# Kernel tuning notes

Hardware: AMD Instinct MI355X
Metric: run time of the kernel (lower is better)

## Reference

```python
import jax, jax.numpy as jnp
import numpy as np

N, E, F_IN, HEADS, C_HEAD, HID, B, NCLS = 20000, 320000, 128, 2, 256, 512, 64, 38
EL = E + N  # edges with self-loops appended


def _bn(x, g, b, eps=1e-5):
    mu = jnp.mean(x, 0)
    var = jnp.mean((x - mu) ** 2, 0)
    return g * (x - mu) * jax.lax.rsqrt(var + eps) + b


def _gcn(x, W, b, src, dst):
    # src/dst already include self-loops; symmetric deg^-1/2 normalization (PyG GCNConv)
    h = x @ W                                             # [N, HID]
    deg = jax.ops.segment_sum(jnp.ones(EL, x.dtype), dst, N)
    norm = jax.lax.rsqrt(jnp.maximum(deg, 1.0))
    coef = norm[src] * norm[dst]                          # [EL]
    agg = jax.ops.segment_sum(h[src] * coef[:, None], dst, N)
    return agg + b


def _gat(x, W, a_src, a_dst, b, src, dst):
    # PyG GATConv, heads=2, concat: alpha = softmax_dst(leaky_relu(a_s.h_src + a_d.h_dst))
    h = (x @ W).reshape(N, HEADS, C_HEAD)
    as_n = jnp.sum(h * a_src, -1)                         # [N, HEADS]
    ad_n = jnp.sum(h * a_dst, -1)
    e = jax.nn.leaky_relu(as_n[src] + ad_n[dst], 0.2)     # [EL, HEADS]
    m = jax.ops.segment_max(e, dst, N)
    ex = jnp.exp(e - m[dst])
    s = jax.ops.segment_sum(ex, dst, N)
    alpha = ex / s[dst]                                   # [EL, HEADS]
    out = jax.ops.segment_sum(h[src] * alpha[:, :, None], dst, N)
    return out.reshape(N, HEADS * C_HEAD) + b


def setup_inputs() -> dict:
    key = jax.random.key(0)
    ks = jax.random.split(key, 40)
    x = jax.random.normal(ks[0], (N, F_IN), jnp.float32)
    edge_index = jax.random.randint(ks[1], (2, E), 0, N, jnp.int32)
    batch = jnp.sort(jax.random.randint(ks[2], (N,), 0, B, jnp.int32))

    def lin(k, fi, fo):
        bound = np.sqrt(6.0 / fi)
        return jax.random.uniform(k, (fi, fo), jnp.float32, -bound, bound)

    d = dict(x=x, edge_index=edge_index, batch=batch)
    # feature transform
    d['ft_W'] = lin(ks[3], F_IN, HID); d['ft_b'] = jnp.zeros(HID)
    d['ft_g'] = jnp.ones(HID); d['ft_be'] = jnp.zeros(HID)
    # GCN block
    d['gcn1_W'] = lin(ks[4], HID, HID); d['gcn1_b'] = jnp.zeros(HID)
    d['gbn1_g'] = jnp.ones(HID); d['gbn1_b'] = jnp.zeros(HID)
    d['gcn2_W'] = lin(ks[5], HID, HID); d['gcn2_b'] = jnp.zeros(HID)
    d['gbn2_g'] = jnp.ones(HID); d['gbn2_b'] = jnp.zeros(HID)
    # GAT block
    abound = np.sqrt(6.0 / HEADS)
    d['gat1_W'] = lin(ks[6], HID, HID)
    d['gat1_as'] = jax.random.uniform(ks[7], (HEADS, C_HEAD), jnp.float32, -abound, abound)
    d['gat1_ad'] = jax.random.uniform(ks[8], (HEADS, C_HEAD), jnp.float32, -abound, abound)
    d['gat1_b'] = jnp.zeros(HID)
    d['abn1_g'] = jnp.ones(HID); d['abn1_b'] = jnp.zeros(HID)
    d['gat2_W'] = lin(ks[9], HID, HID)
    d['gat2_as'] = jax.random.uniform(ks[10], (HEADS, C_HEAD), jnp.float32, -abound, abound)
    d['gat2_ad'] = jax.random.uniform(ks[11], (HEADS, C_HEAD), jnp.float32, -abound, abound)
    d['gat2_b'] = jnp.zeros(HID)
    d['abn2_g'] = jnp.ones(HID); d['abn2_b'] = jnp.zeros(HID)
    # classifier
    d['fc1_W'] = lin(ks[12], 2 * HID, HID); d['fc1_b'] = jnp.zeros(HID)
    d['cbn1_g'] = jnp.ones(HID); d['cbn1_b'] = jnp.zeros(HID)
    d['fc2_W'] = lin(ks[13], HID, HID // 2); d['fc2_b'] = jnp.zeros(HID // 2)
    d['cbn2_g'] = jnp.ones(HID // 2); d['cbn2_b'] = jnp.zeros(HID // 2)
    d['out_W'] = lin(ks[14], HID // 2, NCLS); d['out_b'] = jnp.zeros(NCLS)
    return d


def reference(x, edge_index, batch,
              ft_W, ft_b, ft_g, ft_be,
              gcn1_W, gcn1_b, gbn1_g, gbn1_b, gcn2_W, gcn2_b, gbn2_g, gbn2_b,
              gat1_W, gat1_as, gat1_ad, gat1_b, abn1_g, abn1_b,
              gat2_W, gat2_as, gat2_ad, gat2_b, abn2_g, abn2_b,
              fc1_W, fc1_b, cbn1_g, cbn1_b, fc2_W, fc2_b, cbn2_g, cbn2_b,
              out_W, out_b):
    loop = jnp.arange(N, dtype=edge_index.dtype)
    src = jnp.concatenate([edge_index[0], loop])
    dst = jnp.concatenate([edge_index[1], loop])

    # feature transform: Linear -> BN -> LeakyReLU(0.2)
    h = jax.nn.leaky_relu(_bn(x @ ft_W + ft_b, ft_g, ft_be), 0.2)
    # GCN block
    h = jax.nn.elu(_bn(_gcn(h, gcn1_W, gcn1_b, src, dst), gbn1_g, gbn1_b))
    h = jax.nn.elu(_bn(_gcn(h, gcn2_W, gcn2_b, src, dst), gbn2_g, gbn2_b))
    # GAT block
    h = jax.nn.elu(_bn(_gat(h, gat1_W, gat1_as, gat1_ad, gat1_b, src, dst), abn1_g, abn1_b))
    h = jax.nn.elu(_bn(_gat(h, gat2_W, gat2_as, gat2_ad, gat2_b, src, dst), abn2_g, abn2_b))
    # global mean+max pool over graphs
    cnt = jax.ops.segment_sum(jnp.ones(N, h.dtype), batch, B)
    mean_p = jax.ops.segment_sum(h, batch, B) / jnp.maximum(cnt, 1.0)[:, None]
    max_p = jax.ops.segment_max(h, batch, B)
    p = jnp.concatenate([mean_p, max_p], axis=1)           # [B, 1024]
    # classifier: fc1 -> bn -> fc2 -> bn -> leaky_relu -> out
    z = _bn(p @ fc1_W + fc1_b, cbn1_g, cbn1_b)
    z = _bn(z @ fc2_W + fc2_b, cbn2_g, cbn2_b)
    z = jax.nn.leaky_relu(z, 0.2)
    return z @ out_W + out_b                                # [B, NCLS]
```

## Files before the change

kernel.cpp:

```cpp
#include <hip/hip_runtime.h>

#define N_NODES 20000
#define N_EDGES 320000
#define EDG_ALL (N_EDGES + N_NODES)
#define F_IN 128
#define HID 512
#define NB 64
#define NCLS 38
#define M_PAD2 20480
#define ROW_BLKS 160
#define NBLK_SCAN ((N_NODES + 255) / 256)
#define BN_ROWS 16
#define BN_GRID ((N_NODES + BN_ROWS - 1) / BN_ROWS)
#define NPART 64
#define POOL_SPLIT 4

typedef short bf16x8 __attribute__((ext_vector_type(8)));
typedef float f32x4 __attribute__((ext_vector_type(4)));
typedef _Float16 f16;
typedef _Float16 f16x2 __attribute__((ext_vector_type(2)));
typedef _Float16 f16x8 __attribute__((ext_vector_type(8)));

__device__ inline unsigned short f2bf(float f) {
  union { float f; unsigned u; } v; v.f = f;
  unsigned r = v.u + 0x7FFF + ((v.u >> 16) & 1);
  return (unsigned short)(r >> 16);
}

__device__ inline void split2(float f, unsigned short& h, unsigned short& l) {
  unsigned short hh = f2bf(f);
  union { unsigned u; float f; } vh; vh.u = ((unsigned)hh) << 16;
  h = hh;
  l = f2bf(f - vh.f);
}

__device__ inline void gload16(const void* g, void* l) {
  __builtin_amdgcn_global_load_lds(
      (const __attribute__((address_space(1))) unsigned int*)g,
      (__attribute__((address_space(3))) unsigned int*)l, 16, 0, 0);
}

__device__ inline float lrelu(float v) { return v > 0.f ? v : 0.2f * v; }


__global__ void deg_count(const int* __restrict__ ei, int* __restrict__ deg) {
  int e = blockIdx.x * blockDim.x + threadIdx.x;
  if (e >= EDG_ALL) return;
  int d = (e < N_EDGES) ? ei[N_EDGES + e] : (e - N_EDGES);
  atomicAdd(&deg[d], 1);
}

__global__ void scan_p1(const int* __restrict__ deg, int* __restrict__ bsum) {
  __shared__ int sh[256];
  int b = blockIdx.x, t = threadIdx.x, i = b * 256 + t;
  sh[t] = (i < N_NODES) ? deg[i] : 0;
  __syncthreads();
  for (int o = 128; o > 0; o >>= 1) {
    if (t < o) sh[t] += sh[t + o];
    __syncthreads();
  }
  if (t == 0) bsum[b] = sh[0];
}

__global__ void scan_p2(const int* __restrict__ bsum, int* __restrict__ boff) {
  __shared__ int sh[128];
  int t = threadIdx.x;
  sh[t] = (t < NBLK_SCAN) ? bsum[t] : 0;
  __syncthreads();
  for (int o = 1; o < 128; o <<= 1) {
    int v = (t >= o) ? sh[t - o] : 0;
    __syncthreads();
    sh[t] += v;
    __syncthreads();
  }
  boff[t] = (t == 0) ? 0 : sh[t - 1];
}

__global__ void scan_p3(const int* __restrict__ deg, const int* __restrict__ boff,
                        int* __restrict__ row_ptr) {
  __shared__ int sh[256];
  int b = blockIdx.x, t = threadIdx.x, i = b * 256 + t;
  sh[t] = (i < N_NODES) ? deg[i] : 0;
  __syncthreads();
  for (int o = 1; o < 256; o <<= 1) {
    int v = (t >= o) ? sh[t - o] : 0;
    __syncthreads();
    sh[t] += v;
    __syncthreads();
  }
  if (i < N_NODES) row_ptr[i + 1] = boff[b] + sh[t];
  if (i == 0) row_ptr[0] = 0;
}

__global__ void compute_norm(const int* __restrict__ deg, float* __restrict__ norm) {
  int i = blockIdx.x * blockDim.x + threadIdx.x;
  if (i >= N_NODES) return;
  norm[i] = rsqrtf(fmaxf((float)deg[i], 1.f));
}

__global__ void fill_csr(const int* __restrict__ ei, int* __restrict__ cursor,
                         int* __restrict__ csr_src) {
  int e = blockIdx.x * blockDim.x + threadIdx.x;
  if (e >= EDG_ALL) return;
  int s, d;
  if (e < N_EDGES) { s = ei[e]; d = ei[N_EDGES + e]; }
  else { s = d = e - N_EDGES; }
  int pos = atomicAdd(&cursor[d], 1);
  csr_src[pos] = s;
}


__global__ void conv_split4(const float* __restrict__ in, unsigned short* __restrict__ hi,
                            unsigned short* __restrict__ lo, int n4) {
  int i = blockIdx.x * blockDim.x + threadIdx.x;
  if (i >= n4) return;
  float4 v = ((const float4*)in)[i];
  ushort4 h, l;
  split2(v.x, h.x, l.x); split2(v.y, h.y, l.y);
  split2(v.z, h.z, l.z); split2(v.w, h.w, l.w);
  ((ushort4*)hi)[i] = h;
  ((ushort4*)lo)[i] = l;
}

__global__ __launch_bounds__(256) void wtrans_split(const float* __restrict__ W,
                                                    unsigned short* __restrict__ WTh,
                                                    unsigned short* __restrict__ WTl,
                                                    int K, int N) {
  __shared__ float sh[32][33];
  int k0 = blockIdx.y * 32, n0 = blockIdx.x * 32;
  int r = threadIdx.x >> 5, c = threadIdx.x & 31;
#pragma unroll
  for (int i = 0; i < 4; ++i)
    sh[r + 8 * i][c] = W[(size_t)(k0 + r + 8 * i) * N + n0 + c];
  __syncthreads();
#pragma unroll
  for (int i = 0; i < 4; ++i) {
    unsigned short h, l;
    split2(sh[c][r + 8 * i], h, l);
    WTh[(size_t)(n0 + r + 8 * i) * K + k0 + c] = h;
    WTl[(size_t)(n0 + r + 8 * i) * K + k0 + c] = l;
  }
}

__global__ __launch_bounds__(256) void ftrans(const float* __restrict__ W,
                                              float* __restrict__ WT, int K, int N) {
  __shared__ float sh[32][33];
  int k0 = blockIdx.y * 32, n0 = blockIdx.x * 32;
  int r = threadIdx.x >> 5, c = threadIdx.x & 31;
#pragma unroll
  for (int i = 0; i < 4; ++i) {
    int k = k0 + r + 8 * i, n = n0 + c;
    sh[r + 8 * i][c] = (k < K && n < N) ? W[(size_t)k * N + n] : 0.f;
  }
  __syncthreads();
#pragma unroll
  for (int i = 0; i < 4; ++i) {
    int n = n0 + r + 8 * i, k = k0 + c;
    if (n < N && k < K) WT[(size_t)n * K + k] = sh[c][r + 8 * i];
  }
}


template <int K, typename OT>
__global__ __launch_bounds__(256) void mm_split(const unsigned short* __restrict__ Ah,
                                                const unsigned short* __restrict__ Al,
                                                const unsigned short* __restrict__ Bh,
                                                const unsigned short* __restrict__ Bl,
                                                const float* __restrict__ bias,
                                                OT* __restrict__ C) {
  __shared__ unsigned short AsH[4096], AsL[4096], BsH[4096], BsL[4096];
  const int t = threadIdx.x;
  const int wid = t >> 6, l = t & 63;
  const int bid = blockIdx.x;
  const int g = bid >> 5, w = bid & 31;
  const int row0 = (g * 8 + (w & 7)) * 128;
  const int col0 = (w >> 3) * 128;
  const int wm = wid >> 1, wn = wid & 1;

  f32x4 acc[4][4];
#pragma unroll
  for (int m = 0; m < 4; ++m)
#pragma unroll
    for (int n = 0; n < 4; ++n)
#pragma unroll
      for (int q = 0; q < 4; ++q) acc[m][n][q] = 0.f;

  const size_t aoff = (size_t)(row0 + wid * 32 + (l >> 2)) * K + (l & 3) * 8;
  const size_t boff = (size_t)(col0 + wid * 32 + (l >> 2)) * K + (l & 3) * 8;
  const unsigned short* gAh0 = Ah + aoff; const unsigned short* gAh1 = gAh0 + (size_t)16 * K;
  const unsigned short* gAl0 = Al + aoff; const unsigned short* gAl1 = gAl0 + (size_t)16 * K;
  const unsigned short* gBh0 = Bh + boff; const unsigned short* gBh1 = gBh0 + (size_t)16 * K;
  const unsigned short* gBl0 = Bl + boff; const unsigned short* gBl1 = gBl0 + (size_t)16 * K;
  unsigned short* lAh0 = &AsH[(wid * 2 + 0) * 512];
  unsigned short* lAh1 = &AsH[(wid * 2 + 1) * 512];
  unsigned short* lAl0 = &AsL[(wid * 2 + 0) * 512];
  unsigned short* lAl1 = &AsL[(wid * 2 + 1) * 512];
  unsigned short* lBh0 = &BsH[(wid * 2 + 0) * 512];
  unsigned short* lBh1 = &BsH[(wid * 2 + 1) * 512];
  unsigned short* lBl0 = &BsL[(wid * 2 + 0) * 512];
  unsigned short* lBl1 = &BsL[(wid * 2 + 1) * 512];

  const int lr = l & 15, kq = (l >> 4) * 8;

  for (int kt = 0; kt < K / 32; ++kt) {
    const int ko = kt * 32;
    gload16(gAh0 + ko, lAh0);
    gload16(gAh1 + ko, lAh1);
    gload16(gAl0 + ko, lAl0);
    gload16(gAl1 + ko, lAl1);
    gload16(gBh0 + ko, lBh0);
    gload16(gBh1 + ko, lBh1);
    gload16(gBl0 + ko, lBl0);
    gload16(gBl1 + ko, lBl1);
    __syncthreads();
    bf16x8 ah[4], al[4], bh[4], bl[4];
#pragma unroll
    for (int m = 0; m < 4; ++m) {
      int ro = (wm * 64 + m * 16 + lr) * 32 + kq;
      ah[m] = *(const bf16x8*)&AsH[ro];
      al[m] = *(const bf16x8*)&AsL[ro];
    }
#pragma unroll
    for (int n = 0; n < 4; ++n) {
      int ro = (wn * 64 + n * 16 + lr) * 32 + kq;
      bh[n] = *(const bf16x8*)&BsH[ro];
      bl[n] = *(const bf16x8*)&BsL[ro];
    }
#pragma unroll
    for (int m = 0; m < 4; ++m)
#pragma unroll
      for (int n = 0; n < 4; ++n) {
        acc[m][n] = __builtin_amdgcn_mfma_f32_16x16x32_bf16(ah[m], bh[n], acc[m][n], 0, 0, 0);
        acc[m][n] = __builtin_amdgcn_mfma_f32_16x16x32_bf16(al[m], bh[n], acc[m][n], 0, 0, 0);
        acc[m][n] = __builtin_amdgcn_mfma_f32_16x16x32_bf16(ah[m], bl[n], acc[m][n], 0, 0, 0);
      }
    __syncthreads();
  }

  const int lg = l >> 4;
#pragma unroll
  for (int m = 0; m < 4; ++m) {
    int row = row0 + wm * 64 + m * 16 + lg * 4;
#pragma unroll
    for (int n = 0; n < 4; ++n) {
      int col = col0 + wn * 64 + n * 16 + lr;
      float bv = bias ? bias[col] : 0.f;
#pragma unroll
      for (int j = 0; j < 4; ++j)
        C[(size_t)(row + j) * HID + col] = (OT)(acc[m][n][j] + bv);
    }
  }
}


__global__ __launch_bounds__(256) void colstats(const f16* __restrict__ X, int n,
                                                float* __restrict__ part) {
  int t = threadIdx.x;
  int r0 = blockIdx.x * BN_ROWS;
  int r1 = min(r0 + BN_ROWS, n);
  float s0 = 0, q0 = 0, s1 = 0, q1 = 0;
  const f16x2* X2 = (const f16x2*)X;
  for (int r = r0; r < r1; ++r) {
    f16x2 v = X2[(size_t)r * 256 + t];
    float a = (float)v.x, b = (float)v.y;
    s0 += a; q0 += a * a;
    s1 += b; q1 += b * b;
  }
  float* pb = part + (size_t)(blockIdx.x & (NPART - 1)) * 1024;
  atomicAdd(&pb[2 * t], s0);
  atomicAdd(&pb[2 * t + 1], s1);
  atomicAdd(&pb[HID + 2 * t], q0);
  atomicAdd(&pb[HID + 2 * t + 1], q1);
}

__global__ __launch_bounds__(256) void stats_comb(const float* __restrict__ part,
                                                  float* __restrict__ stats) {
  int j = blockIdx.x * 256 + threadIdx.x;
  float s = 0.f;
#pragma unroll 8
  for (int k = 0; k < NPART; ++k) s += part[(size_t)k * 1024 + j];
  stats[j] = s;
}

__global__ __launch_bounds__(256) void bn_act(f16* __restrict__ X, int n,
                                              const float* __restrict__ stats,
                                              const float* __restrict__ g,
                                              const float* __restrict__ b, int act,
                                              unsigned short* __restrict__ hio,
                                              unsigned short* __restrict__ loo,
                                              int writeX) {
  int t = threadIdx.x;
  int r0 = blockIdx.x * BN_ROWS;
  int r1 = min(r0 + BN_ROWS, n);
  float invn = 1.f / (float)n;
  float mu0 = stats[2 * t] * invn, mu1 = stats[2 * t + 1] * invn;
  float v0 = stats[HID + 2 * t] * invn - mu0 * mu0;
  float v1 = stats[HID + 2 * t + 1] * invn - mu1 * mu1;
  float2 gg = ((const float2*)g)[t];
  float2 bb = ((const float2*)b)[t];
  float sc0 = gg.x * rsqrtf(v0 + 1e-5f);
  float sc1 = gg.y * rsqrtf(v1 + 1e-5f);
  f16x2* X2 = (f16x2*)X;
  ushort2* H2 = (ushort2*)hio;
  ushort2* L2p = (ushort2*)loo;
  for (int r = r0; r < r1; ++r) {
    f16x2 xv = X2[(size_t)r * 256 + t];
    float y0 = sc0 * ((float)xv.x - mu0) + bb.x;
    float y1 = sc1 * ((float)xv.y - mu1) + bb.y;
    if (act == 1) {
      y0 = y0 > 0.f ? y0 : 0.2f * y0;
      y1 = y1 > 0.f ? y1 : 0.2f * y1;
    } else {
      y0 = y0 > 0.f ? y0 : expm1f(y0);
      y1 = y1 > 0.f ? y1 : expm1f(y1);
    }
    unsigned short h0, l0, h1, l1;
    split2(y0, h0, l0);
    split2(y1, h1, l1);
    ushort2 hh; hh.x = h0; hh.y = h1;
    ushort2 ll; ll.x = l0; ll.y = l1;
    H2[(size_t)r * 256 + t] = hh;
    L2p[(size_t)r * 256 + t] = ll;
    if (writeX) {
      f16x2 yv; yv.x = (f16)y0; yv.y = (f16)y1;
      X2[(size_t)r * 256 + t] = yv;
    }
  }
}


__global__ __launch_bounds__(256) void gcn_agg_w(
    const f16* __restrict__ h, const int* __restrict__ row_ptr,
    const int* __restrict__ csr_src, const float* __restrict__ norm,
    const float* __restrict__ bias, f16* __restrict__ out) {
  int node = blockIdx.x * 4 + (threadIdx.x >> 6);
  int l = threadIdx.x & 63;
  int beg = row_ptr[node], end = row_ptr[node + 1];
  float ni = norm[node];
  const f16x8* h8 = (const f16x8*)h;
  float acc[8] = {};
  int e = beg;
  for (; e + 4 <= end; e += 4) {
    int s0 = csr_src[e], s1 = csr_src[e + 1], s2 = csr_src[e + 2], s3 = csr_src[e + 3];
    float c0 = norm[s0] * ni, c1 = norm[s1] * ni, c2 = norm[s2] * ni, c3 = norm[s3] * ni;
    f16x8 v0 = h8[(size_t)s0 * 64 + l];
    f16x8 v1 = h8[(size_t)s1 * 64 + l];
    f16x8 v2 = h8[(size_t)s2 * 64 + l];
    f16x8 v3 = h8[(size_t)s3 * 64 + l];
#pragma unroll
    for (int k = 0; k < 8; ++k)
      acc[k] += c0 * (float)v0[k] + c1 * (float)v1[k] + c2 * (float)v2[k] + c3 * (float)v3[k];
  }
  for (; e < end; ++e) {
    int s = csr_src[e];
    float c = norm[s] * ni;
    f16x8 v = h8[(size_t)s * 64 + l];
#pragma unroll
    for (int k = 0; k < 8; ++k) acc[k] += c * (float)v[k];
  }
  float4 b0 = ((const float4*)bias)[l * 2];
  float4 b1 = ((const float4*)bias)[l * 2 + 1];
  f16x8 o;
  o[0] = (f16)(acc[0] + b0.x); o[1] = (f16)(acc[1] + b0.y);
  o[2] = (f16)(acc[2] + b0.z); o[3] = (f16)(acc[3] + b0.w);
  o[4] = (f16)(acc[4] + b1.x); o[5] = (f16)(acc[5] + b1.y);
  o[6] = (f16)(acc[6] + b1.z); o[7] = (f16)(acc[7] + b1.w);
  ((f16x8*)out)[(size_t)node * 64 + l] = o;
}


__device__ inline float wave_sum(float v) {
#pragma unroll
  for (int o = 32; o > 0; o >>= 1) v += __shfl_down(v, o);
  return v;
}

__global__ __launch_bounds__(256) void gat_prep_h(
    const f16* __restrict__ h, const float* __restrict__ a_src,
    const float* __restrict__ a_dst, float* __restrict__ asn, float* __restrict__ adn) {
  int i = blockIdx.x;
  int t = threadIdx.x;
  f16x2 hv = ((const f16x2*)h)[(size_t)i * 256 + t];
  float2 as2 = ((const float2*)a_src)[t];
  float2 ad2 = ((const float2*)a_dst)[t];
  float h0 = (float)hv.x, h1 = (float)hv.y;
  float s = h0 * as2.x + h1 * as2.y;
  float d = h0 * ad2.x + h1 * ad2.y;
  s = wave_sum(s); d = wave_sum(d);
  __shared__ float red[4][2];
  int w = t >> 6;
  if ((t & 63) == 0) { red[w][0] = s; red[w][1] = d; }
  __syncthreads();
  if (t == 0) {
    asn[2 * i]     = red[0][0] + red[1][0];
    asn[2 * i + 1] = red[2][0] + red[3][0];
    adn[2 * i]     = red[0][1] + red[1][1];
    adn[2 * i + 1] = red[2][1] + red[3][1];
  }
}

__global__ __launch_bounds__(256) void gat_agg_w(
    const f16* __restrict__ h, const int* __restrict__ row_ptr,
    const int* __restrict__ csr_src, const float* __restrict__ asn,
    const float* __restrict__ adn, const float* __restrict__ bias,
    f16* __restrict__ out) {
  int node = blockIdx.x * 4 + (threadIdx.x >> 6);
  int l = threadIdx.x & 63;
  int hl = l & 31;
  int hd = (l >> 5) & 1;
  int beg = row_ptr[node], end = row_ptr[node + 1];
  float aD = adn[2 * node + hd];

  float m = -3.4e38f;
  for (int e = beg + hl; e < end; e += 32) {
    int s = csr_src[e];
    m = fmaxf(m, lrelu(asn[2 * s + hd] + aD));
  }
#pragma unroll
  for (int o = 16; o > 0; o >>= 1) m = fmaxf(m, __shfl_xor(m, o));
  float M = m;

  const f16x8* h8 = (const f16x8*)h;
  float acc[8] = {};
  float sw = 0.f;
  int e = beg;
  for (; e + 4 <= end; e += 4) {
    int s0 = csr_src[e], s1 = csr_src[e + 1], s2 = csr_src[e + 2], s3 = csr_src[e + 3];
    float u0 = expf(lrelu(asn[2 * s0 + hd] + aD) - M);
    float u1 = expf(lrelu(asn[2 * s1 + hd] + aD) - M);
    float u2 = expf(lrelu(asn[2 * s2 + hd] + aD) - M);
    float u3 = expf(lrelu(asn[2 * s3 + hd] + aD) - M);
    sw += u0 + u1 + u2 + u3;
    f16x8 v0 = h8[(size_t)s0 * 64 + l];
    f16x8 v1 = h8[(size_t)s1 * 64 + l];
    f16x8 v2 = h8[(size_t)s2 * 64 + l];
    f16x8 v3 = h8[(size_t)s3 * 64 + l];
#pragma unroll
    for (int k = 0; k < 8; ++k)
      acc[k] += u0 * (float)v0[k] + u1 * (float)v1[k] + u2 * (float)v2[k] + u3 * (float)v3[k];
  }
  for (; e < end; ++e) {
    int s = csr_src[e];
    float u = expf(lrelu(asn[2 * s + hd] + aD) - M);
    sw += u;
    f16x8 v = h8[(size_t)s * 64 + l];
#pragma unroll
    for (int k = 0; k < 8; ++k) acc[k] += u * (float)v[k];
  }
  float iS = 1.f / sw;
  float4 b0 = ((const float4*)bias)[l * 2];
  float4 b1 = ((const float4*)bias)[l * 2 + 1];
  f16x8 o;
  o[0] = (f16)(acc[0] * iS + b0.x); o[1] = (f16)(acc[1] * iS + b0.y);
  o[2] = (f16)(acc[2] * iS + b0.z); o[3] = (f16)(acc[3] * iS + b0.w);
  o[4] = (f16)(acc[4] * iS + b1.x); o[5] = (f16)(acc[5] * iS + b1.y);
  o[6] = (f16)(acc[6] * iS + b1.z); o[7] = (f16)(acc[7] * iS + b1.w);
  ((f16x8*)out)[(size_t)node * 64 + l] = o;
}


__global__ void graph_starts(const int* __restrict__ batch, int* __restrict__ start) {
  int i = blockIdx.x * blockDim.x + threadIdx.x;
  if (i >= N_NODES) return;
  int b = batch[i];
  int bp = (i == 0) ? -1 : batch[i - 1];
  for (int g = bp + 1; g <= b; ++g) start[g] = i;
  if (i == N_NODES - 1) {
    for (int g = b + 1; g <= NB; ++g) start[g] = N_NODES;
  }
}

__global__ __launch_bounds__(256) void pool_part(const f16* __restrict__ h,
                                                 const int* __restrict__ start,
                                                 float* __restrict__ pp_sum,
                                                 float* __restrict__ pp_max) {
  int b = blockIdx.x, ch = blockIdx.y, t = threadIdx.x;
  int s = start[b], e = start[b + 1];
  int len = e - s;
  int c0 = s + (len * ch) / POOL_SPLIT;
  int c1 = s + (len * (ch + 1)) / POOL_SPLIT;
  const f16x2* h2 = (const f16x2*)h;
  float s0 = 0.f, s1 = 0.f, m0 = -3.4e38f, m1 = -3.4e38f;
  int r = c0;
  for (; r + 2 <= c1; r += 2) {
    f16x2 v0 = h2[(size_t)(r + 0) * 256 + t];
    f16x2 v1 = h2[(size_t)(r + 1) * 256 + t];
    float a0 = (float)v0.x, a1 = (float)v0.y, b0 = (float)v1.x, b1 = (float)v1.y;
    s0 += a0 + b0; s1 += a1 + b1;
    m0 = fmaxf(m0, fmaxf(a0, b0));
    m1 = fmaxf(m1, fmaxf(a1, b1));
  }
  for (; r < c1; ++r) {
    f16x2 v = h2[(size_t)r * 256 + t];
    float a0 = (float)v.x, a1 = (float)v.y;
    s0 += a0; s1 += a1;
    m0 = fmaxf(m0, a0); m1 = fmaxf(m1, a1);
  }
  size_t base = ((size_t)b * POOL_SPLIT + ch) * HID;
  pp_sum[base + 2 * t] = s0;
  pp_sum[base + 2 * t + 1] = s1;
  pp_max[base + 2 * t] = m0;
  pp_max[base + 2 * t + 1] = m1;
}

__global__ __launch_bounds__(512) void pool_comb(const float* __restrict__ pp_sum,
                                                 const float* __restrict__ pp_max,
                                                 const int* __restrict__ start,
                                                 float* __restrict__ p) {
  int b = blockIdx.x, t = threadIdx.x;
  float sum = 0.f, mx = -3.4e38f;
#pragma unroll
  for (int ch = 0; ch < POOL_SPLIT; ++ch) {
    sum += pp_sum[((size_t)b * POOL_SPLIT + ch) * HID + t];
    mx = fmaxf(mx, pp_max[((size_t)b * POOL_SPLIT + ch) * HID + t]);
  }
  float cnt = (float)(start[b + 1] - start[b]);
  p[b * 1024 + t] = sum / fmaxf(cnt, 1.f);
  p[b * 1024 + 512 + t] = mx;
}


__global__ __launch_bounds__(256) void fc_wave(const float* __restrict__ A,
                                               const float* __restrict__ WT,
                                               const float* __restrict__ bias,
                                               float* __restrict__ C, int K, int Ncol) {
  int r = blockIdx.x;
  int wid = threadIdx.x >> 6, l = threadIdx.x & 63;
  int c = blockIdx.y * 4 + wid;
  if (c >= Ncol) return;
  const float* a = A + (size_t)r * K;
  const float* w = WT + (size_t)c * K;
  float s = 0.f;
  for (int k = l; k < K; k += 64) s += a[k] * w[k];
#pragma unroll
  for (int o = 32; o > 0; o >>= 1) s += __shfl_down(s, o);
  if (l == 0) C[(size_t)r * Ncol + c] = s + bias[c];
}

__global__ void bn_small(float* __restrict__ X, int R, int C,
                         const float* __restrict__ g, const float* __restrict__ b, int act) {
  int c = blockIdx.x * blockDim.x + threadIdx.x;
  if (c >= C) return;
  float s = 0.f, q = 0.f;
  for (int r = 0; r < R; ++r) {
    float v = X[r * C + c];
    s += v; q += v * v;
  }
  float mu = s / R;
  float var = q / R - mu * mu;
  float sc = g[c] * rsqrtf(var + 1e-5f);
  float bb = b[c];
  for (int r = 0; r < R; ++r) {
    float v = sc * (X[r * C + c] - mu) + bb;
    if (act == 1) v = v > 0.f ? v : 0.2f * v;
    X[r * C + c] = v;
  }
}


extern "C" void kernel_launch(void* const* d_in, const int* in_sizes, int n_in,
                              void* d_out, int out_size, void* d_ws, size_t ws_size,
                              hipStream_t stream) {
  const float* x      = (const float*)d_in[0];
  const int*   ei     = (const int*)d_in[1];
  const int*   batch  = (const int*)d_in[2];
  const float* ft_W   = (const float*)d_in[3];
  const float* ft_b   = (const float*)d_in[4];
  const float* ft_g   = (const float*)d_in[5];
  const float* ft_be  = (const float*)d_in[6];
  const float* gcn1_W = (const float*)d_in[7];
  const float* gcn1_b = (const float*)d_in[8];
  const float* gbn1_g = (const float*)d_in[9];
  const float* gbn1_b = (const float*)d_in[10];
  const float* gcn2_W = (const float*)d_in[11];
  const float* gcn2_b = (const float*)d_in[12];
  const float* gbn2_g = (const float*)d_in[13];
  const float* gbn2_b = (const float*)d_in[14];
  const float* gat1_W = (const float*)d_in[15];
  const float* gat1_as= (const float*)d_in[16];
  const float* gat1_ad= (const float*)d_in[17];
  const float* gat1_b = (const float*)d_in[18];
  const float* abn1_g = (const float*)d_in[19];
  const float* abn1_b = (const float*)d_in[20];
  const float* gat2_W = (const float*)d_in[21];
  const float* gat2_as= (const float*)d_in[22];
  const float* gat2_ad= (const float*)d_in[23];
  const float* gat2_b = (const float*)d_in[24];
  const float* abn2_g = (const float*)d_in[25];
  const float* abn2_b = (const float*)d_in[26];
  const float* fc1_W  = (const float*)d_in[27];
  const float* fc1_b  = (const float*)d_in[28];
  const float* cbn1_g = (const float*)d_in[29];
  const float* cbn1_b = (const float*)d_in[30];
  const float* fc2_W  = (const float*)d_in[31];
  const float* fc2_b  = (const float*)d_in[32];
  const float* cbn2_g = (const float*)d_in[33];
  const float* cbn2_b = (const float*)d_in[34];
  const float* out_W  = (const float*)d_in[35];
  const float* out_b  = (const float*)d_in[36];

  char* ws = (char*)d_ws;
  size_t off = 0;
  auto alloc = [&](size_t bytes) -> void* {
    void* p = ws + off;
    off = (off + bytes + 255) & ~(size_t)255;
    return p;
  };

  float* buf0 = (float*)alloc((size_t)M_PAD2 * HID * 4);
  float* buf1 = (float*)alloc((size_t)M_PAD2 * HID * 4);
  unsigned short* ahi = (unsigned short*)alloc((size_t)M_PAD2 * HID * 2);
  unsigned short* alo = (unsigned short*)alloc((size_t)M_PAD2 * HID * 2);
  unsigned short* wh_ft = (unsigned short*)alloc((size_t)HID * F_IN * 2);
  unsigned short* wl_ft = (unsigned short*)alloc((size_t)HID * F_IN * 2);
  unsigned short* wh_g1 = (unsigned short*)alloc((size_t)HID * HID * 2);
  unsigned short* wl_g1 = (unsigned short*)alloc((size_t)HID * HID * 2);
  unsigned short* wh_g2 = (unsigned short*)alloc((size_t)HID * HID * 2);
  unsigned short* wl_g2 = (unsigned short*)alloc((size_t)HID * HID * 2);
  unsigned short* wh_a1 = (unsigned short*)alloc((size_t)HID * HID * 2);
  unsigned short* wl_a1 = (unsigned short*)alloc((size_t)HID * HID * 2);
  unsigned short* wh_a2 = (unsigned short*)alloc((size_t)HID * HID * 2);
  unsigned short* wl_a2 = (unsigned short*)alloc((size_t)HID * HID * 2);
  float* fc1t = (float*)alloc((size_t)512 * 1024 * 4);
  float* fc2t = (float*)alloc((size_t)256 * 512 * 4);
  float* outt = (float*)alloc((size_t)NCLS * 256 * 4);
  int*   row_ptr = (int*)alloc((N_NODES + 1) * 4);
  int*   cursor  = (int*)alloc(N_NODES * 4);
  int*   deg     = (int*)alloc(N_NODES * 4);
  int*   csr_src = (int*)alloc(EDG_ALL * 4);
  float* norm    = (float*)alloc(N_NODES * 4);
  float* asn     = (float*)alloc(N_NODES * 2 * 4);
  float* adn     = (float*)alloc(N_NODES * 2 * 4);
  float* stats   = (float*)alloc(1024 * 4);
  float* spart   = (float*)alloc((size_t)NPART * 1024 * 4);
  int*   bsum    = (int*)alloc(128 * 4);
  int*   boff    = (int*)alloc(128 * 4);
  int*   start   = (int*)alloc((NB + 1) * 4);
  float* p       = (float*)alloc(NB * 1024 * 4);
  float* pp_sum  = (float*)alloc((size_t)NB * POOL_SPLIT * HID * 4);
  float* pp_max  = (float*)alloc((size_t)NB * POOL_SPLIT * HID * 4);
  float* z1      = (float*)alloc(NB * HID * 4);
  float* z2      = (float*)alloc(NB * 256 * 4);
  unsigned short* xhi = (unsigned short*)buf0;
  unsigned short* xlo = xhi + (size_t)M_PAD2 * F_IN;
  f16* xbuf = (f16*)buf0;
  f16* hbuf = (f16*)buf1;

  const dim3 blk256(256);
  const dim3 mmGrid(ROW_BLKS * 4);
  const int aggGrid = N_NODES / 4;

#define BN_BLOCK(XBUF, G, B, ACT, WX)                                            \
  hipMemsetAsync(spart, 0, (size_t)NPART * 1024 * 4, stream);                    \
  colstats<<<BN_GRID, blk256, 0, stream>>>(XBUF, N_NODES, spart);                \
  stats_comb<<<4, blk256, 0, stream>>>(spart, stats);                            \
  bn_act<<<BN_GRID, blk256, 0, stream>>>(XBUF, N_NODES, stats, G, B, ACT, ahi, alo, WX);

  hipMemsetAsync(deg, 0, N_NODES * 4, stream);
  deg_count<<<(EDG_ALL + 255) / 256, blk256, 0, stream>>>(ei, deg);
  scan_p1<<<NBLK_SCAN, blk256, 0, stream>>>(deg, bsum);
  scan_p2<<<1, 128, 0, stream>>>(bsum, boff);
  scan_p3<<<NBLK_SCAN, blk256, 0, stream>>>(deg, boff, row_ptr);
  compute_norm<<<(N_NODES + 255) / 256, blk256, 0, stream>>>(deg, norm);
  hipMemcpyAsync(cursor, row_ptr, N_NODES * 4, hipMemcpyDeviceToDevice, stream);
  fill_csr<<<(EDG_ALL + 255) / 256, blk256, 0, stream>>>(ei, cursor, csr_src);

  wtrans_split<<<dim3(HID / 32, F_IN / 32), blk256, 0, stream>>>(ft_W, wh_ft, wl_ft, F_IN, HID);
  wtrans_split<<<dim3(HID / 32, HID / 32), blk256, 0, stream>>>(gcn1_W, wh_g1, wl_g1, HID, HID);
  wtrans_split<<<dim3(HID / 32, HID / 32), blk256, 0, stream>>>(gcn2_W, wh_g2, wl_g2, HID, HID);
  wtrans_split<<<dim3(HID / 32, HID / 32), blk256, 0, stream>>>(gat1_W, wh_a1, wl_a1, HID, HID);
  wtrans_split<<<dim3(HID / 32, HID / 32), blk256, 0, stream>>>(gat2_W, wh_a2, wl_a2, HID, HID);
  ftrans<<<dim3(512 / 32, 1024 / 32), blk256, 0, stream>>>(fc1_W, fc1t, 1024, 512);
  ftrans<<<dim3(256 / 32, 512 / 32), blk256, 0, stream>>>(fc2_W, fc2t, 512, 256);
  ftrans<<<dim3((NCLS + 31) / 32, 256 / 32), blk256, 0, stream>>>(out_W, outt, 256, NCLS);

  conv_split4<<<(N_NODES * F_IN / 4 + 255) / 256, blk256, 0, stream>>>(x, xhi, xlo, N_NODES * F_IN / 4);
  mm_split<F_IN, f16><<<mmGrid, blk256, 0, stream>>>(xhi, xlo, wh_ft, wl_ft, ft_b, hbuf);
  BN_BLOCK(hbuf, ft_g, ft_be, 1, 0)

  mm_split<HID, f16><<<mmGrid, blk256, 0, stream>>>(ahi, alo, wh_g1, wl_g1, nullptr, hbuf);
  gcn_agg_w<<<aggGrid, blk256, 0, stream>>>(hbuf, row_ptr, csr_src, norm, gcn1_b, xbuf);
  BN_BLOCK(xbuf, gbn1_g, gbn1_b, 2, 0)

  mm_split<HID, f16><<<mmGrid, blk256, 0, stream>>>(ahi, alo, wh_g2, wl_g2, nullptr, hbuf);
  gcn_agg_w<<<aggGrid, blk256, 0, stream>>>(hbuf, row_ptr, csr_src, norm, gcn2_b, xbuf);
  BN_BLOCK(xbuf, gbn2_g, gbn2_b, 2, 0)

  mm_split<HID, f16><<<mmGrid, blk256, 0, stream>>>(ahi, alo, wh_a1, wl_a1, nullptr, hbuf);
  gat_prep_h<<<N_NODES, blk256, 0, stream>>>(hbuf, gat1_as, gat1_ad, asn, adn);
  gat_agg_w<<<aggGrid, blk256, 0, stream>>>(hbuf, row_ptr, csr_src, asn, adn, gat1_b, xbuf);
  BN_BLOCK(xbuf, abn1_g, abn1_b, 2, 0)

  mm_split<HID, f16><<<mmGrid, blk256, 0, stream>>>(ahi, alo, wh_a2, wl_a2, nullptr, hbuf);
  gat_prep_h<<<N_NODES, blk256, 0, stream>>>(hbuf, gat2_as, gat2_ad, asn, adn);
  gat_agg_w<<<aggGrid, blk256, 0, stream>>>(hbuf, row_ptr, csr_src, asn, adn, gat2_b, xbuf);
  BN_BLOCK(xbuf, abn2_g, abn2_b, 2, 1)

  graph_starts<<<(N_NODES + 255) / 256, blk256, 0, stream>>>(batch, start);
  pool_part<<<dim3(NB, POOL_SPLIT), blk256, 0, stream>>>(xbuf, start, pp_sum, pp_max);
  pool_comb<<<NB, dim3(512), 0, stream>>>(pp_sum, pp_max, start, p);

  fc_wave<<<dim3(NB, 128), blk256, 0, stream>>>(p, fc1t, fc1_b, z1, 1024, 512);
  bn_small<<<2, blk256, 0, stream>>>(z1, NB, 512, cbn1_g, cbn1_b, 0);
  fc_wave<<<dim3(NB, 64), blk256, 0, stream>>>(z1, fc2t, fc2_b, z2, 512, 256);
  bn_small<<<1, blk256, 0, stream>>>(z2, NB, 256, cbn2_g, cbn2_b, 1);
  fc_wave<<<dim3(NB, 10), blk256, 0, stream>>>(z2, outt, out_b, (float*)d_out, 256, NCLS);

#undef BN_BLOCK
  (void)in_sizes; (void)n_in; (void)out_size; (void)ws_size;
}
```

Baseline: 787.1 us.

## Double-buffer LDS tiles in split-bf16 GEMM to overlap loads with MFMA

Adds a second LDS buffer for each of the A/B high/low tiles. The next k-tile is prefetched into the alternate buffer while MFMAs run on the current one, and the trailing barrier is removed so there is one sync per iteration. The goal is to hide global-to-LDS latency behind compute in the GEMM kernels. LDS usage doubles to 64KB per block, which may reduce occupancy. Correctness depends on gload16 being an async LDS load that the next barrier's waitcnt covers.

Result: slower. 805.7 us (+2.4%).

```diff
diff --git a/kernel.cpp b/kernel.cpp
--- a/kernel.cpp
+++ b/kernel.cpp
@@ -168,7 +168,7 @@
                                                 const unsigned short* __restrict__ Bl,
                                                 const float* __restrict__ bias,
                                                 OT* __restrict__ C) {
-  __shared__ unsigned short AsH[4096], AsL[4096], BsH[4096], BsL[4096];
+  __shared__ unsigned short AsH[2][4096], AsL[2][4096], BsH[2][4096], BsL[2][4096];
   const int t = threadIdx.x;
   const int wid = t >> 6, l = t & 63;
   const int bid = blockIdx.x;
@@ -191,40 +191,50 @@
   const unsigned short* gAl0 = Al + aoff; const unsigned short* gAl1 = gAl0 + (size_t)16 * K;
   const unsigned short* gBh0 = Bh + boff; const unsigned short* gBh1 = gBh0 + (size_t)16 * K;
   const unsigned short* gBl0 = Bl + boff; const unsigned short* gBl1 = gBl0 + (size_t)16 * K;
-  unsigned short* lAh0 = &AsH[(wid * 2 + 0) * 512];
-  unsigned short* lAh1 = &AsH[(wid * 2 + 1) * 512];
-  unsigned short* lAl0 = &AsL[(wid * 2 + 0) * 512];
-  unsigned short* lAl1 = &AsL[(wid * 2 + 1) * 512];
-  unsigned short* lBh0 = &BsH[(wid * 2 + 0) * 512];
-  unsigned short* lBh1 = &BsH[(wid * 2 + 1) * 512];
-  unsigned short* lBl0 = &BsL[(wid * 2 + 0) * 512];
-  unsigned short* lBl1 = &BsL[(wid * 2 + 1) * 512];
+  const int c0 = (wid * 2 + 0) * 512;
+  const int c1 = (wid * 2 + 1) * 512;
 
   const int lr = l & 15, kq = (l >> 4) * 8;
-
-  for (int kt = 0; kt < K / 32; ++kt) {
-    const int ko = kt * 32;
-    gload16(gAh0 + ko, lAh0);
-    gload16(gAh1 + ko, lAh1);
-    gload16(gAl0 + ko, lAl0);
-    gload16(gAl1 + ko, lAl1);
-    gload16(gBh0 + ko, lBh0);
-    gload16(gBh1 + ko, lBh1);
-    gload16(gBl0 + ko, lBl0);
-    gload16(gBl1 + ko, lBl1);
+  const int NT = K / 32;
+
+  {
+    gload16(gAh0, &AsH[0][c0]);
+    gload16(gAh1, &AsH[0][c1]);
+    gload16(gAl0, &AsL[0][c0]);
+    gload16(gAl1, &AsL[0][c1]);
+    gload16(gBh0, &BsH[0][c0]);
+    gload16(gBh1, &BsH[0][c1]);
+    gload16(gBl0, &BsL[0][c0]);
+    gload16(gBl1, &BsL[0][c1]);
+  }
+
+  for (int kt = 0; kt < NT; ++kt) {
+    const int cur = kt & 1;
     __syncthreads();
+    if (kt + 1 < NT) {
+      const int ko = (kt + 1) * 32;
+      const int nxt = cur ^ 1;
+      gload16(gAh0 + ko, &AsH[nxt][c0]);
+      gload16(gAh1 + ko, &AsH[nxt][c1]);
+      gload16(gAl0 + ko, &AsL[nxt][c0]);
+      gload16(gAl1 + ko, &AsL[nxt][c1]);
+      gload16(gBh0 + ko, &BsH[nxt][c0]);
+      gload16(gBh1 + ko, &BsH[nxt][c1]);
+      gload16(gBl0 + ko, &BsL[nxt][c0]);
+      gload16(gBl1 + ko, &BsL[nxt][c1]);
+    }
     bf16x8 ah[4], al[4], bh[4], bl[4];
 #pragma unroll
     for (int m = 0; m < 4; ++m) {
       int ro = (wm * 64 + m * 16 + lr) * 32 + kq;
-      ah[m] = *(const bf16x8*)&AsH[ro];
-      al[m] = *(const bf16x8*)&AsL[ro];
+      ah[m] = *(const bf16x8*)&AsH[cur][ro];
+      al[m] = *(const bf16x8*)&AsL[cur][ro];
     }
 #pragma unroll
     for (int n = 0; n < 4; ++n) {
       int ro = (wn * 64 + n * 16 + lr) * 32 + kq;
-      bh[n] = *(const bf16x8*)&BsH[ro];
-      bl[n] = *(const bf16x8*)&BsL[ro];
+      bh[n] = *(const bf16x8*)&BsH[cur][ro];
+      bl[n] = *(const bf16x8*)&BsL[cur][ro];
     }
 #pragma unroll
     for (int m = 0; m < 4; ++m)
@@ -234,7 +244,6 @@
         acc[m][n] = __builtin_amdgcn_mfma_f32_16x16x32_bf16(al[m], bh[n], acc[m][n], 0, 0, 0);
         acc[m][n] = __builtin_amdgcn_mfma_f32_16x16x32_bf16(ah[m], bl[n], acc[m][n], 0, 0, 0);
       }
-    __syncthreads();
   }
 
   const int lg = l >> 4;
```
